# Kernel tuning notes

Hardware: AMD Instinct MI355X
Metric: run time of the kernel (lower is better)

Reference implementation:

```python
import jax, jax.numpy as jnp
import numpy as np

N = 100000      # nodes
E = 625000      # edges
F_IN = 128      # num_features
C = 32          # num_classes


def setup_inputs() -> dict:
    key = jax.random.key(0)
    k1, k2, k3, k4, k5 = jax.random.split(key, 5)
    x = jax.random.normal(k1, (N, F_IN), dtype=jnp.float32)
    edge_index = jax.random.randint(k2, (2, E), 0, N, dtype=jnp.int64)
    s = 1.0 / np.sqrt(F_IN)
    # PyG SAGEConv: lin_l (applied to aggregated neighbors, with bias), lin_r (applied to self, no bias)
    W_l = jax.random.uniform(k3, (C, F_IN), dtype=jnp.float32, minval=-s, maxval=s)
    b_l = jax.random.uniform(k4, (C,), dtype=jnp.float32, minval=-s, maxval=s)
    W_r = jax.random.uniform(k5, (C, F_IN), dtype=jnp.float32, minval=-s, maxval=s)
    return {"x": x, "edge_index": edge_index, "W_l": W_l, "b_l": b_l, "W_r": W_r}


def reference(x, edge_index, W_l, b_l, W_r):
    src, dst = edge_index[0], edge_index[1]
    # mean aggregation of source-node features at destination nodes
    msg_sum = jax.ops.segment_sum(x[src], dst, num_segments=N)            # [N, F]
    deg = jax.ops.segment_sum(jnp.ones((E,), x.dtype), dst, num_segments=N)
    agg = msg_sum / jnp.maximum(deg, 1.0)[:, None]
    # SAGEConv: lin_l(agg) + lin_r(x)
    h = agg @ W_l.T + b_l + x @ W_r.T                                     # [N, C]
    h = jax.nn.relu(h)
    # dropout is identity in eval mode
    return jax.nn.log_softmax(h, axis=1)
```

## Files before the change

kernel.cpp:

```cpp
#include <hip/hip_runtime.h>
#include <hip/hip_fp16.h>
#include <math.h>

#define F_IN 128
#define NCLS 32
#define ZC   64
#define CAP  64
#define NPART 8
#define WROWS 64

typedef __attribute__((ext_vector_type(8))) short short8v;
typedef __attribute__((ext_vector_type(4))) float f32x4;

__device__ __forceinline__ unsigned int pk2(float lo, float hi) {
    unsigned int a = __float_as_uint(lo), b = __float_as_uint(hi);
    a = (a + 0x7fffu + ((a >> 16) & 1u)) >> 16;
    b = (b + 0x7fffu + ((b >> 16) & 1u)) >> 16;
    return a | (b << 16);
}
__device__ __forceinline__ uint4 pack8(float4 a, float4 b) {
    return make_uint4(pk2(a.x, a.y), pk2(a.z, a.w), pk2(b.x, b.y), pk2(b.z, b.w));
}

__global__ __launch_bounds__(256) void init_kernel(const float* __restrict__ Wl,
                                                   const float* __restrict__ Wr,
                                                   unsigned short* __restrict__ wb,
                                                   int* __restrict__ cnt, int N) {
    int t = threadIdx.x;
    int i = blockIdx.x * 256 + t;
    if (i < N) cnt[i] = 0;
    if (blockIdx.x == 0) {
        #pragma unroll
        for (int p = 0; p < 4; ++p) {
            int idx = t + p * 256;
            int row = idx >> 4;
            int q   = idx & 15;
            const float* srcW = (row < NCLS) ? (Wl + row * F_IN) : (Wr + (row - NCLS) * F_IN);
            float4 a = *(const float4*)(srcW + q * 8);
            float4 b = *(const float4*)(srcW + q * 8 + 4);
            *(uint4*)(wb + row * F_IN + q * 8) = pack8(a, b);
        }
    }
}

__global__ __launch_bounds__(256) void proj_kernel(const float* __restrict__ x,
                                                   const unsigned short* __restrict__ wb,
                                                   __half* __restrict__ z, int N) {
    int t = threadIdx.x;
    int node0 = blockIdx.x * 64;
    int wave = t >> 6;
    int lane = t & 63;
    int l15  = lane & 15;
    int koff = (lane >> 4) * 8;

    int row  = node0 + wave * 16 + l15;
    int safe = (row < N) ? row : (N - 1);
    const float* xr = x + (size_t)safe * F_IN + koff;
    const unsigned short* wr = wb + l15 * F_IN + koff;

    f32x4 acc[4] = {{0.f,0.f,0.f,0.f},{0.f,0.f,0.f,0.f},{0.f,0.f,0.f,0.f},{0.f,0.f,0.f,0.f}};

    #pragma unroll
    for (int ks = 0; ks < 4; ++ks) {
        float4 xa = *(const float4*)(xr + ks * 32);
        float4 xb = *(const float4*)(xr + ks * 32 + 4);
        uint4 ap = pack8(xa, xb);
        short8v a = *reinterpret_cast<short8v*>(&ap);
        #pragma unroll
        for (int ct = 0; ct < 4; ++ct) {
            short8v b = *reinterpret_cast<const short8v*>(wr + ct * 16 * F_IN + ks * 32);
            acc[ct] = __builtin_amdgcn_mfma_f32_16x16x32_bf16(a, b, acc[ct], 0, 0, 0);
        }
    }

    int r0 = (lane >> 4) * 4;
    #pragma unroll
    for (int ct = 0; ct < 4; ++ct) {
        #pragma unroll
        for (int r = 0; r < 4; ++r) {
            int node = node0 + wave * 16 + r0 + r;
            if (node < N) z[(size_t)node * ZC + ct * 16 + l15] = __float2half(acc[ct][r]);
        }
    }
}

__global__ __launch_bounds__(256) void fill_kernel(const void* __restrict__ ei,
                                                   int* __restrict__ cnt,
                                                   int* __restrict__ col,
                                                   int E, int N, int span) {
    const unsigned int* u32 = (const unsigned int*)ei;
    unsigned int aa = 0;
    #pragma unroll
    for (int j = 0; j < 16; ++j) aa |= u32[2 * j + 1];
    int is64 = (aa == 0u);

    int part = blockIdx.x & (NPART - 1);
    int e0 = ((blockIdx.x >> 3) * 256 + threadIdx.x) * 4;
    if (e0 >= E) return;
    int lo = part * span;
    int hi = lo + span; if (hi > N) hi = N;
    int ecnt = (E - e0 >= 4) ? 4 : (E - e0);

    int d[4];
    if (is64) {
        const long long* dp = (const long long*)ei + E + e0;
        if (ecnt == 4) {
            longlong2 d01 = *(const longlong2*)dp, d23 = *(const longlong2*)(dp + 2);
            d[0]=(int)d01.x; d[1]=(int)d01.y; d[2]=(int)d23.x; d[3]=(int)d23.y;
        } else {
            for (int j = 0; j < ecnt; ++j) d[j] = (int)dp[j];
        }
    } else {
        const int* dp = (const int*)ei + E + e0;
        if (ecnt == 4) {
            int4 dv = *(const int4*)dp;
            d[0]=dv.x; d[1]=dv.y; d[2]=dv.z; d[3]=dv.w;
        } else {
            for (int j = 0; j < ecnt; ++j) d[j] = dp[j];
        }
    }

    for (int j = 0; j < ecnt; ++j) {
        if (d[j] >= lo && d[j] < hi) {
            int sv = is64 ? (int)((const long long*)ei)[e0 + j]
                          : ((const int*)ei)[e0 + j];
            if ((unsigned)sv >= (unsigned)N) sv = 0;
            int pos = atomicAdd(&cnt[d[j]], 1);
            if (pos < CAP) col[(size_t)d[j] * CAP + pos] = sv;
        }
    }
}

__global__ __launch_bounds__(256) void finish_kernel(const __half* __restrict__ z,
                                                     const int* __restrict__ col,
                                                     const int* __restrict__ cnt,
                                                     const float* __restrict__ bl,
                                                     float* __restrict__ out, int N) {
    int gid = blockIdx.x * 256 + threadIdx.x;
    int node = gid >> 5;
    int c = gid & 31;
    if (node >= N) return;

    int deg = cnt[node];
    int m = (deg < CAP) ? deg : CAP;
    const int* cb = col + (size_t)node * CAP;
    float selfz = __half2float(z[(size_t)node * ZC + NCLS + c]);
    float bias  = bl[c];

    float a[8] = {};
    for (int base = 0; base < m; base += 8) {
        int4 n0 = *(const int4*)(cb + base);
        int4 n1 = *(const int4*)(cb + base + 4);
        int idx[8] = {n0.x, n0.y, n0.z, n0.w, n1.x, n1.y, n1.z, n1.w};
        #pragma unroll
        for (int k = 0; k < 8; ++k) {
            bool ok = (base + k < m);
            int s = ok ? idx[k] : 0;
            float v = __half2float(z[(size_t)s * ZC + c]);
            a[k] += ok ? v : 0.f;
        }
    }
    float acc = ((a[0] + a[1]) + (a[2] + a[3])) + ((a[4] + a[5]) + (a[6] + a[7]));

    float inv = 1.0f / fmaxf((float)deg, 1.0f);
    float h = acc * inv + bias + selfz;
    h = fmaxf(h, 0.f);

    float mx = h;
    #pragma unroll
    for (int o = 16; o >= 1; o >>= 1) mx = fmaxf(mx, __shfl_xor(mx, o));
    float p = h - mx;
    float ex = __expf(p);
    float s = ex;
    #pragma unroll
    for (int o = 16; o >= 1; o >>= 1) s += __shfl_xor(s, o);

    out[(size_t)node * NCLS + c] = p - __logf(s);
}

__global__ void detect_i64_kernel(const unsigned int* __restrict__ ei, int* __restrict__ flag) {
    if (blockIdx.x == 0 && threadIdx.x == 0) {
        unsigned int acc = 0;
        #pragma unroll
        for (int i = 0; i < 64; ++i) acc |= ei[2 * i + 1];
        *flag = (acc == 0u) ? 1 : 0;
    }
}

__global__ __launch_bounds__(256) void scatter_kernel(const float* __restrict__ x,
                                                      const void* __restrict__ ei,
                                                      const int* __restrict__ flag,
                                                      float* __restrict__ msg,
                                                      float* __restrict__ deg, int E, int N) {
    long long gid = (long long)blockIdx.x * blockDim.x + threadIdx.x;
    int e = (int)(gid >> 5);
    if (e >= E) return;
    int c = (int)(gid & 31);
    int is64 = *flag;
    int src = is64 ? (int)((const long long*)ei)[e] : ((const int*)ei)[e];
    int dst = is64 ? (int)((const long long*)ei)[(size_t)E + e] : ((const int*)ei)[(size_t)E + e];
    if ((unsigned)src >= (unsigned)N || (unsigned)dst >= (unsigned)N) return;
    float4 v = *(const float4*)(x + (size_t)src * F_IN + (c << 2));
    float* m = msg + (size_t)dst * F_IN + (c << 2);
    atomicAdd(m + 0, v.x);
    atomicAdd(m + 1, v.y);
    atomicAdd(m + 2, v.z);
    atomicAdd(m + 3, v.w);
    if (c == 0) atomicAdd(deg + dst, 1.0f);
}

__global__ __launch_bounds__(256) void apply_kernel(const float* __restrict__ x,
                                                    const float* __restrict__ msg,
                                                    const float* __restrict__ degf,
                                                    const float* __restrict__ Wl,
                                                    const float* __restrict__ bl,
                                                    const float* __restrict__ Wr,
                                                    float* __restrict__ out, int N) {
    int n = blockIdx.x * 256 + threadIdx.x;
    if (n >= N) return;
    float inv = 1.0f / fmaxf(degf[n], 1.0f);
    float acc[NCLS];
    #pragma unroll
    for (int c = 0; c < NCLS; ++c) acc[c] = bl[c];
    const float* xr = x + (size_t)n * F_IN;
    const float* mr = msg + (size_t)n * F_IN;
    for (int kb = 0; kb < F_IN; kb += 4) {
        float4 xv = *(const float4*)(xr + kb);
        float4 mv = *(const float4*)(mr + kb);
        float b0 = mv.x * inv, b1 = mv.y * inv, b2 = mv.z * inv, b3 = mv.w * inv;
        #pragma unroll
        for (int c = 0; c < NCLS; ++c) {
            float4 wl = *(const float4*)(Wl + c * F_IN + kb);
            float4 wr = *(const float4*)(Wr + c * F_IN + kb);
            acc[c] += b0 * wl.x + b1 * wl.y + b2 * wl.z + b3 * wl.w
                    + xv.x * wr.x + xv.y * wr.y + xv.z * wr.z + xv.w * wr.w;
        }
    }
    float mx = 0.0f;
    #pragma unroll
    for (int c = 0; c < NCLS; ++c) { acc[c] = fmaxf(acc[c], 0.0f); mx = fmaxf(mx, acc[c]); }
    float s = 0.0f;
    #pragma unroll
    for (int c = 0; c < NCLS; ++c) s += __expf(acc[c] - mx);
    float lg = __logf(s);
    float* o = out + (size_t)n * NCLS;
    #pragma unroll
    for (int q = 0; q < NCLS; q += 4) {
        float4 w = make_float4(acc[q] - mx - lg, acc[q + 1] - mx - lg,
                               acc[q + 2] - mx - lg, acc[q + 3] - mx - lg);
        *(float4*)(o + q) = w;
    }
}

extern "C" void kernel_launch(void* const* d_in, const int* in_sizes, int n_in,
                              void* d_out, int out_size, void* d_ws, size_t ws_size,
                              hipStream_t stream) {
    const float* x  = (const float*)d_in[0];
    const void*  ei = d_in[1];
    const float* Wl = (const float*)d_in[2];
    const float* bl = (const float*)d_in[3];
    const float* Wr = (const float*)d_in[4];

    int N = in_sizes[0] / F_IN;
    int E = in_sizes[1] / 2;
    int span = (N + NPART - 1) / NPART;

    size_t need = (size_t)N * ZC * 2 + (size_t)N * 4 + (size_t)N * CAP * 4
                + (size_t)WROWS * F_IN * 2;

    if (ws_size >= need) {
        __half* z   = (__half*)d_ws;
        int*    cnt = (int*)((char*)d_ws + (size_t)N * ZC * 2);
        int*    col = cnt + N;
        unsigned short* wb = (unsigned short*)(col + (size_t)N * CAP);
        float*  outp = (float*)d_out;

        int T  = (N + 63) / 64;
        int FU = ((E + 1023) / 1024) * NPART;

        init_kernel<<<(N + 255) / 256, 256, 0, stream>>>(Wl, Wr, wb, cnt, N);
        proj_kernel<<<T, 256, 0, stream>>>(x, wb, z, N);
        fill_kernel<<<FU, 256, 0, stream>>>(ei, cnt, col, E, N, span);
        long long tot = (long long)N * 32;
        finish_kernel<<<(int)((tot + 255) / 256), 256, 0, stream>>>(z, col, cnt, bl,
                                                                    outp, N);
    } else {
        float* msg  = (float*)d_ws;
        float* deg  = msg + (size_t)N * F_IN;
        int*   flag = (int*)(deg + N);

        hipMemsetAsync(d_ws, 0, ((size_t)N * F_IN + N) * 4, stream);
        detect_i64_kernel<<<1, 64, 0, stream>>>((const unsigned int*)ei, flag);

        long long tot = (long long)E * 32;
        scatter_kernel<<<(int)((tot + 255) / 256), 256, 0, stream>>>(x, ei, flag, msg, deg, E, N);
        apply_kernel<<<(N + 255) / 256, 256, 0, stream>>>(x, msg, deg, Wl, bl, Wr,
                                                          (float*)d_out, N);
    }
}
```

Measured before the change: 83.65 us.

## Stage x and weights in padded LDS for projection; move count zeroing into proj

The projection kernel now loads each block's 64 rows of x with coalesced full-row float4 reads, converts them to bf16 and stores them in padded shared memory alongside the bf16 weight matrix. The MFMA operands are then read from LDS instead of from strided global reads. Zeroing of the per-node count array moves from init_kernel into proj_kernel, so init_kernel shrinks to a single block that only converts weights. This is meant to improve global-load coalescing and cut the size of the init launch, at the cost of about 34KB of LDS per block and a barrier, which may lower occupancy.

```diff
diff --git a/kernel.cpp b/kernel.cpp
--- a/kernel.cpp
+++ b/kernel.cpp
@@ -7,6 +7,7 @@
 #define ZC   64
 #define CAP  64
 #define NPART 8
+#define PADW 136
 #define WROWS 64
 
 typedef __attribute__((ext_vector_type(8))) short short8v;
@@ -24,51 +25,67 @@
 
 __global__ __launch_bounds__(256) void init_kernel(const float* __restrict__ Wl,
                                                    const float* __restrict__ Wr,
-                                                   unsigned short* __restrict__ wb,
-                                                   int* __restrict__ cnt, int N) {
+                                                   unsigned short* __restrict__ wb) {
     int t = threadIdx.x;
-    int i = blockIdx.x * 256 + t;
-    if (i < N) cnt[i] = 0;
-    if (blockIdx.x == 0) {
-        #pragma unroll
-        for (int p = 0; p < 4; ++p) {
-            int idx = t + p * 256;
-            int row = idx >> 4;
-            int q   = idx & 15;
-            const float* srcW = (row < NCLS) ? (Wl + row * F_IN) : (Wr + (row - NCLS) * F_IN);
-            float4 a = *(const float4*)(srcW + q * 8);
-            float4 b = *(const float4*)(srcW + q * 8 + 4);
-            *(uint4*)(wb + row * F_IN + q * 8) = pack8(a, b);
-        }
+    #pragma unroll
+    for (int p = 0; p < 4; ++p) {
+        int idx = t + p * 256;
+        int row = idx >> 4;
+        int q   = idx & 15;
+        const float* srcW = (row < NCLS) ? (Wl + row * F_IN) : (Wr + (row - NCLS) * F_IN);
+        float4 a = *(const float4*)(srcW + q * 8);
+        float4 b = *(const float4*)(srcW + q * 8 + 4);
+        *(uint4*)(wb + row * F_IN + q * 8) = pack8(a, b);
     }
 }
 
 __global__ __launch_bounds__(256) void proj_kernel(const float* __restrict__ x,
                                                    const unsigned short* __restrict__ wb,
-                                                   __half* __restrict__ z, int N) {
+                                                   __half* __restrict__ z,
+                                                   int* __restrict__ cnt, int N) {
+    __shared__ __align__(16) unsigned short xs[64 * PADW];
+    __shared__ __align__(16) unsigned short ws[64 * PADW];
     int t = threadIdx.x;
     int node0 = blockIdx.x * 64;
+
+    if (t < 64) {
+        int n = node0 + t;
+        if (n < N) cnt[n] = 0;
+    }
+
+    #pragma unroll
+    for (int p = 0; p < 4; ++p) {
+        int idx = t + p * 256;
+        int row = idx >> 4;
+        int q   = idx & 15;
+
+        uint4 wv = *(const uint4*)(wb + row * F_IN + q * 8);
+        *(uint4*)(ws + row * PADW + q * 8) = wv;
+
+        int node = node0 + row;
+        int safe = (node < N) ? node : (N - 1);
+        const float* srcX = x + (size_t)safe * F_IN;
+        float4 xa = *(const float4*)(srcX + q * 8);
+        float4 xb = *(const float4*)(srcX + q * 8 + 4);
+        *(uint4*)(xs + row * PADW + q * 8) = pack8(xa, xb);
+    }
+    __syncthreads();
+
     int wave = t >> 6;
     int lane = t & 63;
     int l15  = lane & 15;
     int koff = (lane >> 4) * 8;
 
-    int row  = node0 + wave * 16 + l15;
-    int safe = (row < N) ? row : (N - 1);
-    const float* xr = x + (size_t)safe * F_IN + koff;
-    const unsigned short* wr = wb + l15 * F_IN + koff;
-
     f32x4 acc[4] = {{0.f,0.f,0.f,0.f},{0.f,0.f,0.f,0.f},{0.f,0.f,0.f,0.f},{0.f,0.f,0.f,0.f}};
+    const unsigned short* xrow = xs + (wave * 16 + l15) * PADW + koff;
+    const unsigned short* wrow = ws + l15 * PADW + koff;
 
     #pragma unroll
     for (int ks = 0; ks < 4; ++ks) {
-        float4 xa = *(const float4*)(xr + ks * 32);
-        float4 xb = *(const float4*)(xr + ks * 32 + 4);
-        uint4 ap = pack8(xa, xb);
-        short8v a = *reinterpret_cast<short8v*>(&ap);
+        short8v a = *reinterpret_cast<const short8v*>(xrow + ks * 32);
         #pragma unroll
         for (int ct = 0; ct < 4; ++ct) {
-            short8v b = *reinterpret_cast<const short8v*>(wr + ct * 16 * F_IN + ks * 32);
+            short8v b = *reinterpret_cast<const short8v*>(wrow + ct * 16 * PADW + ks * 32);
             acc[ct] = __builtin_amdgcn_mfma_f32_16x16x32_bf16(a, b, acc[ct], 0, 0, 0);
         }
     }
@@ -278,8 +295,8 @@
         int T  = (N + 63) / 64;
         int FU = ((E + 1023) / 1024) * NPART;
 
-        init_kernel<<<(N + 255) / 256, 256, 0, stream>>>(Wl, Wr, wb, cnt, N);
-        proj_kernel<<<T, 256, 0, stream>>>(x, wb, z, N);
+        init_kernel<<<1, 256, 0, stream>>>(Wl, Wr, wb);
+        proj_kernel<<<T, 256, 0, stream>>>(x, wb, z, cnt, N);
         fill_kernel<<<FU, 256, 0, stream>>>(ei, cnt, col, E, N, span);
         long long tot = (long long)N * 32;
         finish_kernel<<<(int)((tot + 255) / 256), 256, 0, stream>>>(z, col, cnt, bl,
```

Result: faster. 72.81 us (-13.0%).
